# Kernel tuning notes

Hardware: AMD Instinct MI355X
Metric: run time of the kernel (lower is better)

Reference implementation:

```python
import jax, jax.numpy as jnp
import numpy as np
from jax import lax

B, S, F, D, H, L, A = 16, 512, 64, 512, 8, 4, 3
E = D // H  # head_dim = 64

def _gelu(t):
    return jax.nn.gelu(t, approximate=False)  # torch nn.GELU() is exact erf

def _make_masks():
    i = jnp.arange(S)[:, None]
    j = jnp.arange(S)[None, :]
    d = jnp.abs(i - j)
    ms = []
    for h in range(min(5, H)):
        dil = 2 ** h
        ms.append((d <= dil) | (d % (2 ** (h + 1)) == 0))
    m = jnp.stack(ms)  # [5,S,S] bool
    idx = jnp.minimum(jnp.arange(H), m.shape[0] - 1)
    return m[idx]  # [H,S,S]

MASKS = _make_masks()

def _ln(x, g, b, eps=1e-5):
    mu = jnp.mean(x, -1, keepdims=True)
    var = jnp.mean((x - mu) ** 2, -1, keepdims=True)
    return (x - mu) * lax.rsqrt(var + eps) * g + b

def _conv1d(x_ncw, w, b):
    y = lax.conv_general_dilated(x_ncw, w, (1,), [(1, 1)],
                                 dimension_numbers=("NCH", "OIH", "NCH"))
    return y + b[None, :, None]

def _attn(x, Wq, bq, Wk, bk, Wv, bv, Wo, bo):
    # x: [B,S,D]; Wq/Wk/Wv: [H,E,D] (stacked per-head Linear weights)
    q = jnp.einsum("bsd,hed->bhse", x, Wq) + bq[None, :, None, :]
    k = jnp.einsum("bsd,hed->bhse", x, Wk) + bk[None, :, None, :]
    v = jnp.einsum("bsd,hed->bhse", x, Wv) + bv[None, :, None, :]
    s = jnp.einsum("bhse,bhte->bhst", q, k) / (E ** 0.5)
    s = jnp.where(MASKS[None], s, -jnp.inf)  # log-sparse masked_fill
    p = jax.nn.softmax(s, axis=-1)
    o = jnp.einsum("bhst,bhte->bhse", p, v)
    o = o.transpose(0, 2, 1, 3).reshape(x.shape[0], x.shape[1], D)  # concat heads
    return o @ Wo.T + bo

def _forward(x, conv1_w, conv1_b, conv2_w, conv2_b, emb_w, emb_b, pos,
             Wq, bq, Wk, bk, Wv, bv, Wo, bo, ln1_g, ln1_b, ln2_g, ln2_b,
             W1, b1, W2, b2, lnf_g, lnf_b,
             a1_w, a1_b, a2_w, a2_b, a3_w, a3_b, a4_w, a4_b,
             c1_w, c1_b, c2_w, c2_b, c3_w, c3_b, c4_w, c4_b):
    # feature extractor: two conv1d+GELU over time axis
    h0 = _gelu(_conv1d(x.transpose(0, 2, 1), conv1_w, conv1_b))
    h0 = _gelu(_conv1d(h0, conv2_w, conv2_b)).transpose(0, 2, 1)  # [B,S,D]
    z = h0 @ emb_w.T + emb_b + pos[:, :S]  # input embedding + positional
    for l in range(L):  # PyraFormer blocks (pre-norm residual)
        z = z + _attn(_ln(z, ln1_g[l], ln1_b[l]),
                      Wq[l], bq[l], Wk[l], bk[l], Wv[l], bv[l], Wo[l], bo[l])
        h = _ln(z, ln2_g[l], ln2_b[l])
        z = z + (_gelu(h @ W1[l].T + b1[l]) @ W2[l].T + b2[l])
    z = _ln(z, lnf_g, lnf_b)
    feat = z[:, -1, :]  # last timestep features

    def head(f, layers):
        (w1, bb1), (w2, bb2), (w3, bb3), (w4, bb4) = layers
        f = _gelu(f @ w1.T + bb1)
        f = _gelu(f @ w2.T + bb2)
        f = _gelu(f @ w3.T + bb3)
        return f @ w4.T + bb4

    policy = head(feat, [(a1_w, a1_b), (a2_w, a2_b), (a3_w, a3_b), (a4_w, a4_b)])
    value = head(feat, [(c1_w, c1_b), (c2_w, c2_b), (c3_w, c3_b), (c4_w, c4_b)])
    return policy, value

def setup_inputs() -> dict:
    key = jax.random.key(0)
    ks = iter(jax.random.split(key, 64))
    r = lambda shape, s=0.05: jax.random.normal(next(ks), shape, jnp.float32) * s
    return {
        "x": jax.random.normal(next(ks), (B, S, F), jnp.float32),
        "conv1_w": r((D // 2, F, 3)), "conv1_b": jnp.zeros((D // 2,)),
        "conv2_w": r((D, D // 2, 3)), "conv2_b": jnp.zeros((D,)),
        "emb_w": r((D, D)), "emb_b": jnp.zeros((D,)),
        "pos": r((1, S, D), 0.02),
        "Wq": r((L, H, E, D)), "bq": jnp.zeros((L, H, E)),
        "Wk": r((L, H, E, D)), "bk": jnp.zeros((L, H, E)),
        "Wv": r((L, H, E, D)), "bv": jnp.zeros((L, H, E)),
        "Wo": r((L, D, D)), "bo": jnp.zeros((L, D)),
        "ln1_g": jnp.ones((L, D)), "ln1_b": jnp.zeros((L, D)),
        "ln2_g": jnp.ones((L, D)), "ln2_b": jnp.zeros((L, D)),
        "W1": r((L, 4 * D, D)), "b1": jnp.zeros((L, 4 * D)),
        "W2": r((L, D, 4 * D)), "b2": jnp.zeros((L, D)),
        "lnf_g": jnp.ones((D,)), "lnf_b": jnp.zeros((D,)),
        "a1_w": r((128, D)), "a1_b": jnp.zeros((128,)),
        "a2_w": r((256, 128)), "a2_b": jnp.zeros((256,)),
        "a3_w": r((57, 256)), "a3_b": jnp.zeros((57,)),
        "a4_w": r((A, 57)), "a4_b": jnp.zeros((A,)),
        "c1_w": r((128, D)), "c1_b": jnp.zeros((128,)),
        "c2_w": r((256, 128)), "c2_b": jnp.zeros((256,)),
        "c3_w": r((57, 256)), "c3_b": jnp.zeros((57,)),
        "c4_w": r((1, 57)), "c4_b": jnp.zeros((1,)),
    }

def reference(x, conv1_w, conv1_b, conv2_w, conv2_b, emb_w, emb_b, pos,
              Wq, bq, Wk, bk, Wv, bv, Wo, bo, ln1_g, ln1_b, ln2_g, ln2_b,
              W1, b1, W2, b2, lnf_g, lnf_b,
              a1_w, a1_b, a2_w, a2_b, a3_w, a3_b, a4_w, a4_b,
              c1_w, c1_b, c2_w, c2_b, c3_w, c3_b, c4_w, c4_b):
    return _forward(x, conv1_w, conv1_b, conv2_w, conv2_b, emb_w, emb_b, pos,
                    Wq, bq, Wk, bk, Wv, bv, Wo, bo, ln1_g, ln1_b, ln2_g, ln2_b,
                    W1, b1, W2, b2, lnf_g, lnf_b,
                    a1_w, a1_b, a2_w, a2_b, a3_w, a3_b, a4_w, a4_b,
                    c1_w, c1_b, c2_w, c2_b, c3_w, c3_b, c4_w, c4_b)
```

## Files before the change

### kernel.cpp

```cpp
#include <hip/hip_runtime.h>
#include <hip/hip_bf16.h>
#include <cstdint>

typedef __attribute__((ext_vector_type(8))) short bf16x8;
typedef __attribute__((ext_vector_type(4))) float f32x4;
typedef unsigned short u16;

#define DEV __device__ __forceinline__

DEV float b2f(u16 u) {
  union { unsigned int i; float f; } v; v.i = ((unsigned int)u) << 16; return v.f;
}
DEV u16 f2b(float f) {
  __hip_bfloat16 h = __float2bfloat16(f);
  return *reinterpret_cast<u16*>(&h);
}
DEV float erf_fast(float x) {
  float ax = fabsf(x);
  float t = __builtin_amdgcn_rcpf(fmaf(0.3275911f, ax, 1.0f));
  float p = t * fmaf(t, fmaf(t, fmaf(t, fmaf(t, 1.061405429f, -1.453152027f),
                                     1.421413741f), -0.284496736f), 0.254829592f);
  float r = fmaf(-p, __expf(-ax * ax), 1.0f);
  return copysignf(r, x);
}
DEV float gelu_f(float x) { return 0.5f * x * (1.0f + erf_fast(x * 0.70710678118654752f)); }

DEV void async_cp16(const u16* g, u16* l) {
  __builtin_amdgcn_global_load_lds(
      (const __attribute__((address_space(1))) void*)g,
      (__attribute__((address_space(3))) void*)l, 16, 0, 0);
}

__global__ void probe_kernel(const unsigned int* __restrict__ g, int* __restrict__ flag) {
  if (threadIdx.x == 0 && blockIdx.x == 0) *flag = (*g == 0x3F800000u) ? 1 : 0;
}

struct CvtArgs {
  const void* src[42];
  unsigned int off[43];
};

struct alignas(16) U8v { u16 u[8]; };
struct alignas(8)  U4v { u16 u[4]; };

__global__ __launch_bounds__(256) void cvt_kernel(CvtArgs a, int n_t, unsigned int total,
                                                  const int* __restrict__ flag,
                                                  u16* __restrict__ dst) {
  unsigned int i8 = (blockIdx.x * 256u + threadIdx.x) * 8u;
  if (i8 >= total) return;
  int t = 0;
  while (t + 1 < n_t && i8 >= a.off[t + 1]) t++;
  unsigned int j = i8 - a.off[t];
  bool in_seg = (i8 + 8 <= a.off[t + 1]) && (i8 + 8 <= total);
  int fp32 = *flag;
  if (fp32) {
    if (in_seg && ((j & 3) == 0)) {
      const float* s = (const float*)a.src[t] + j;
      float4 v0 = *(const float4*)s;
      float4 v1 = *(const float4*)(s + 4);
      U8v o;
      o.u[0] = f2b(v0.x); o.u[1] = f2b(v0.y); o.u[2] = f2b(v0.z); o.u[3] = f2b(v0.w);
      o.u[4] = f2b(v1.x); o.u[5] = f2b(v1.y); o.u[6] = f2b(v1.z); o.u[7] = f2b(v1.w);
      *(U8v*)(dst + i8) = o;
    } else {
      for (int k = 0; k < 8; k++) {
        unsigned int i = i8 + k;
        if (i >= total) break;
        int tt = t;
        while (tt + 1 < n_t && i >= a.off[tt + 1]) tt++;
        dst[i] = f2b(((const float*)a.src[tt])[i - a.off[tt]]);
      }
    }
  } else {
    if (in_seg && ((j & 7) == 0)) {
      *(U8v*)(dst + i8) = *(const U8v*)((const u16*)a.src[t] + j);
    } else {
      for (int k = 0; k < 8; k++) {
        unsigned int i = i8 + k;
        if (i >= total) break;
        int tt = t;
        while (tt + 1 < n_t && i >= a.off[tt + 1]) tt++;
        dst[i] = ((const u16*)a.src[tt])[i - a.off[tt]];
      }
    }
  }
}

__global__ __launch_bounds__(256) void gemm_bt44(
    const u16* __restrict__ A, const u16* __restrict__ W,
    const u16* __restrict__ bias,
    u16* __restrict__ outB, float* __restrict__ outF,
    const u16* __restrict__ pos,
    int N, int K, int mode)
{
  __shared__ __align__(16) u16 As[2][64 * 32];
  __shared__ __align__(16) u16 Bs[2][64 * 32];
  int t = threadIdx.x, l = t & 63, w = t >> 6;
  int wr = w >> 1, wc = w & 1;
  int col = l & 15, quad = l >> 4;
  int q8 = (quad ^ ((col >> 1) & 3)) * 8;
  int m0 = blockIdx.x * 64;
  int n0 = blockIdx.y * 64;

  f32x4 acc[2][2];
#pragma unroll
  for (int i = 0; i < 2; i++)
#pragma unroll
    for (int j = 0; j < 2; j++) acc[i][j] = (f32x4){0.f, 0.f, 0.f, 0.f};

  int ra = t >> 2;
  int ca = (t & 3) ^ ((ra >> 1) & 3);
  const u16* a1 = A + (size_t)(m0 + ra) * K + ca * 8;
  const u16* b1 = W + (size_t)(n0 + ra) * K + ca * 8;

  int nK = K >> 5;
  async_cp16(a1, &As[0][t * 8]);
  async_cp16(b1, &Bs[0][t * 8]);
  for (int ki = 0; ki < nK; ki++) {
    int cur = ki & 1;
    if (ki + 1 < nK) {
      int nxt = cur ^ 1, kt = (ki + 1) << 5;
      async_cp16(a1 + kt, &As[nxt][t * 8]);
      async_cp16(b1 + kt, &Bs[nxt][t * 8]);
      __builtin_amdgcn_s_waitcnt(0x0F72);
    } else {
      __builtin_amdgcn_s_waitcnt(0x0F70);
    }
    __builtin_amdgcn_s_barrier();
    __builtin_amdgcn_sched_barrier(0);
    bf16x8 af[2], bfv[2];
#pragma unroll
    for (int mi = 0; mi < 2; mi++)
      af[mi] = *(const bf16x8*)&As[cur][(wr * 32 + mi * 16 + col) * 32 + q8];
#pragma unroll
    for (int ni = 0; ni < 2; ni++)
      bfv[ni] = *(const bf16x8*)&Bs[cur][(wc * 32 + ni * 16 + col) * 32 + q8];
#pragma unroll
    for (int mi = 0; mi < 2; mi++)
#pragma unroll
      for (int ni = 0; ni < 2; ni++)
        acc[mi][ni] = __builtin_amdgcn_mfma_f32_16x16x32_bf16(bfv[ni], af[mi], acc[mi][ni], 0, 0, 0);
    __builtin_amdgcn_sched_barrier(0);
    __builtin_amdgcn_s_barrier();
  }

  int mBase = m0 + wr * 32, nBase = n0 + wc * 32;
  if (mode == 1) {
#pragma unroll
    for (int mi = 0; mi < 2; mi++) {
      int m = mBase + mi * 16 + col;
      size_t rowOff = (size_t)m * N;
#pragma unroll
      for (int ni = 0; ni < 2; ni++) {
        int n4 = nBase + ni * 16 + quad * 4;
        U4v bb = *(const U4v*)&bias[n4];
        f32x4 v = acc[mi][ni];
        U4v o;
#pragma unroll
        for (int r = 0; r < 4; r++) o.u[r] = f2b(gelu_f(v[r] + b2f(bb.u[r])));
        *(U4v*)&outB[rowOff + n4] = o;
      }
    }
  } else if (mode == 2) {
#pragma unroll
    for (int mi = 0; mi < 2; mi++) {
      int m = mBase + mi * 16 + col;
      size_t rowOff = (size_t)m * N;
#pragma unroll
      for (int ni = 0; ni < 2; ni++) {
        int n4 = nBase + ni * 16 + quad * 4;
        U4v bb = *(const U4v*)&bias[n4];
        f32x4 v = acc[mi][ni];
        float4* p = (float4*)&outF[rowOff + n4];
        float4 zv = *p;
        zv.x += v[0] + b2f(bb.u[0]);
        zv.y += v[1] + b2f(bb.u[1]);
        zv.z += v[2] + b2f(bb.u[2]);
        zv.w += v[3] + b2f(bb.u[3]);
        *p = zv;
      }
    }
  } else {
#pragma unroll
    for (int mi = 0; mi < 2; mi++) {
      int m = mBase + mi * 16 + col;
      int s = m & 511;
      size_t rowOff = (size_t)m * N;
#pragma unroll
      for (int ni = 0; ni < 2; ni++) {
        int n4 = nBase + ni * 16 + quad * 4;
        U4v bb = *(const U4v*)&bias[n4];
        U4v pp = *(const U4v*)&pos[s * 512 + n4];
        f32x4 v = acc[mi][ni];
        float4 zv;
        zv.x = v[0] + b2f(bb.u[0]) + b2f(pp.u[0]);
        zv.y = v[1] + b2f(bb.u[1]) + b2f(pp.u[1]);
        zv.z = v[2] + b2f(bb.u[2]) + b2f(pp.u[2]);
        zv.w = v[3] + b2f(bb.u[3]) + b2f(pp.u[3]);
        *(float4*)&outF[rowOff + n4] = zv;
      }
    }
  }
}

__global__ __launch_bounds__(256) void gemm_bt128x64(
    const u16* __restrict__ A, const u16* __restrict__ W,
    const u16* __restrict__ bias,
    u16* __restrict__ outB, int N, int K)
{
  __shared__ __align__(16) u16 As[2][128 * 32];
  __shared__ __align__(16) u16 Bs[2][64 * 32];
  int t = threadIdx.x, l = t & 63, w = t >> 6;
  int wr = w >> 1, wc = w & 1;
  int col = l & 15, quad = l >> 4;
  int q8 = (quad ^ ((col >> 1) & 3)) * 8;
  int m0 = blockIdx.x * 128;
  int n0 = blockIdx.y * 64;

  f32x4 acc[4][2];
#pragma unroll
  for (int i = 0; i < 4; i++)
#pragma unroll
    for (int j = 0; j < 2; j++) acc[i][j] = (f32x4){0.f, 0.f, 0.f, 0.f};

  int g1i = t, g2i = t + 256;
  int r1 = g1i >> 2, r2 = g2i >> 2;
  int cb1 = (g1i & 3) ^ ((r1 >> 1) & 3);
  int cb2 = (g2i & 3) ^ ((r2 >> 1) & 3);
  int rb = t >> 2;
  int cbb = (t & 3) ^ ((rb >> 1) & 3);
  const u16* a1 = A + (size_t)(m0 + r1) * K + cb1 * 8;
  const u16* a2 = A + (size_t)(m0 + r2) * K + cb2 * 8;
  const u16* b1 = W + (size_t)(n0 + rb) * K + cbb * 8;

  int nK = K >> 5;
  async_cp16(a1, &As[0][g1i * 8]);
  async_cp16(a2, &As[0][g2i * 8]);
  async_cp16(b1, &Bs[0][t * 8]);
  for (int ki = 0; ki < nK; ki++) {
    int cur = ki & 1;
    if (ki + 1 < nK) {
      int nxt = cur ^ 1, kt = (ki + 1) << 5;
      async_cp16(a1 + kt, &As[nxt][g1i * 8]);
      async_cp16(a2 + kt, &As[nxt][g2i * 8]);
      async_cp16(b1 + kt, &Bs[nxt][t * 8]);
      __builtin_amdgcn_s_waitcnt(0x0F73);
    } else {
      __builtin_amdgcn_s_waitcnt(0x0F70);
    }
    __builtin_amdgcn_s_barrier();
    __builtin_amdgcn_sched_barrier(0);
    bf16x8 af[4], bfv[2];
#pragma unroll
    for (int mi = 0; mi < 4; mi++)
      af[mi] = *(const bf16x8*)&As[cur][(wr * 64 + mi * 16 + col) * 32 + q8];
#pragma unroll
    for (int ni = 0; ni < 2; ni++)
      bfv[ni] = *(const bf16x8*)&Bs[cur][(wc * 32 + ni * 16 + col) * 32 + q8];
#pragma unroll
    for (int mi = 0; mi < 4; mi++)
#pragma unroll
      for (int ni = 0; ni < 2; ni++)
        acc[mi][ni] = __builtin_amdgcn_mfma_f32_16x16x32_bf16(bfv[ni], af[mi], acc[mi][ni], 0, 0, 0);
    __builtin_amdgcn_sched_barrier(0);
    __builtin_amdgcn_s_barrier();
  }

  int mBase = m0 + wr * 64, nBase = n0 + wc * 32;
#pragma unroll
  for (int mi = 0; mi < 4; mi++) {
    int m = mBase + mi * 16 + col;
    size_t rowOff = (size_t)m * N;
#pragma unroll
    for (int ni = 0; ni < 2; ni++) {
      int n4 = nBase + ni * 16 + quad * 4;
      U4v bb = *(const U4v*)&bias[n4];
      f32x4 v = acc[mi][ni];
      U4v o;
#pragma unroll
      for (int r = 0; r < 4; r++) o.u[r] = f2b(gelu_f(v[r] + b2f(bb.u[r])));
      *(U4v*)&outB[rowOff + n4] = o;
    }
  }
}

__global__ __launch_bounds__(256) void gemm_qkv256(
    const u16* __restrict__ A,
    const u16* __restrict__ Wq, const u16* __restrict__ Wk, const u16* __restrict__ Wv,
    const u16* __restrict__ bq, const u16* __restrict__ bk, const u16* __restrict__ bv,
    u16* __restrict__ outQ, u16* __restrict__ outK, u16* __restrict__ outVT, int K)
{
  __shared__ __align__(16) u16 As[2][64 * 32];
  __shared__ __align__(16) u16 Bs[2][256 * 32];
  int t = threadIdx.x, l = t & 63, w = t >> 6;
  int wr = w >> 1, wc = w & 1;
  int col = l & 15, quad = l >> 4;
  int q8 = (quad ^ ((col >> 1) & 3)) * 8;
  int m0 = blockIdx.x * 64;
  int sel = blockIdx.y >> 1;
  int n0 = (blockIdx.y & 1) * 256;
  const u16* W = sel == 0 ? Wq : (sel == 1 ? Wk : Wv);
  const u16* bias = sel == 0 ? bq : (sel == 1 ? bk : bv);
  const bool swp = (sel < 2);
  const float scl = sel == 0 ? 0.125f : 1.0f;

  f32x4 acc[2][8];
#pragma unroll
  for (int i = 0; i < 2; i++)
#pragma unroll
    for (int j = 0; j < 8; j++) acc[i][j] = (f32x4){0.f, 0.f, 0.f, 0.f};

  int ra = t >> 2;
  int ca = (t & 3) ^ ((ra >> 1) & 3);
  const u16* a1 = A + (size_t)(m0 + ra) * K + ca * 8;
  const u16* bptr[4];
  int bidx[4];
#pragma unroll
  for (int j = 0; j < 4; j++) {
    int gi = t + 256 * j;
    int rb = gi >> 2;
    int cb = (gi & 3) ^ ((rb >> 1) & 3);
    bptr[j] = W + (size_t)(n0 + rb) * K + cb * 8;
    bidx[j] = gi;
  }

  int nK = K >> 5;
  async_cp16(a1, &As[0][t * 8]);
#pragma unroll
  for (int j = 0; j < 4; j++) async_cp16(bptr[j], &Bs[0][bidx[j] * 8]);
  for (int ki = 0; ki < nK; ki++) {
    int cur = ki & 1;
    if (ki + 1 < nK) {
      int nxt = cur ^ 1, kt = (ki + 1) << 5;
      async_cp16(a1 + kt, &As[nxt][t * 8]);
#pragma unroll
      for (int j = 0; j < 4; j++) async_cp16(bptr[j] + kt, &Bs[nxt][bidx[j] * 8]);
      __builtin_amdgcn_s_waitcnt(0x0F75);
    } else {
      __builtin_amdgcn_s_waitcnt(0x0F70);
    }
    __builtin_amdgcn_s_barrier();
    __builtin_amdgcn_sched_barrier(0);
    bf16x8 af[2], bfv[8];
#pragma unroll
    for (int mi = 0; mi < 2; mi++)
      af[mi] = *(const bf16x8*)&As[cur][(wr * 32 + mi * 16 + col) * 32 + q8];
#pragma unroll
    for (int ni = 0; ni < 8; ni++)
      bfv[ni] = *(const bf16x8*)&Bs[cur][(wc * 128 + ni * 16 + col) * 32 + q8];
    if (swp) {
#pragma unroll
      for (int mi = 0; mi < 2; mi++)
#pragma unroll
        for (int ni = 0; ni < 8; ni++)
          acc[mi][ni] = __builtin_amdgcn_mfma_f32_16x16x32_bf16(bfv[ni], af[mi], acc[mi][ni], 0, 0, 0);
    } else {
#pragma unroll
      for (int mi = 0; mi < 2; mi++)
#pragma unroll
        for (int ni = 0; ni < 8; ni++)
          acc[mi][ni] = __builtin_amdgcn_mfma_f32_16x16x32_bf16(af[mi], bfv[ni], acc[mi][ni], 0, 0, 0);
    }
    __builtin_amdgcn_sched_barrier(0);
    __builtin_amdgcn_s_barrier();
  }

  int mBase = m0 + wr * 32, nBase = n0 + wc * 128;
  if (swp) {
    u16* outB = sel == 0 ? outQ : outK;
#pragma unroll
    for (int mi = 0; mi < 2; mi++) {
      int m = mBase + mi * 16 + col;
      size_t rowOff = (size_t)m * 512;
#pragma unroll
      for (int ni = 0; ni < 8; ni++) {
        int n4 = nBase + ni * 16 + quad * 4;
        U4v bb = *(const U4v*)&bias[n4];
        f32x4 v = acc[mi][ni];
        U4v o;
#pragma unroll
        for (int r = 0; r < 4; r++) o.u[r] = f2b((v[r] + b2f(bb.u[r])) * scl);
        *(U4v*)&outB[rowOff + n4] = o;
      }
    }
  } else {
    int b = m0 >> 9;
    int sB = m0 & 511;
#pragma unroll
    for (int mi = 0; mi < 2; mi++) {
      int s4 = sB + wr * 32 + mi * 16 + quad * 4;
#pragma unroll
      for (int ni = 0; ni < 8; ni++) {
        int n = nBase + ni * 16 + col;
        int h = n >> 6, e = n & 63;
        float bvv = b2f(bias[n]);
        f32x4 v = acc[mi][ni];
        U4v o;
#pragma unroll
        for (int r = 0; r < 4; r++) o.u[r] = f2b(v[r] + bvv);
        *(U4v*)&outVT[((size_t)((b * 8 + h) * 64 + e)) * 512 + s4] = o;
      }
    }
  }
}

__global__ void im2col3_kernel(const u16* __restrict__ src,
                               u16* __restrict__ dst, int C)
{
  int m = blockIdx.x;
  int k = blockIdx.y * blockDim.x + threadIdx.x;
  int ci = k / 3;
  int tap = k - ci * 3;
  int s = m & 511;
  int sp = s + tap - 1;
  u16 val = 0;
  if (sp >= 0 && sp < 512) val = src[(size_t)(m + tap - 1) * C + ci];
  dst[(size_t)m * (3 * C) + k] = val;
}

__global__ __launch_bounds__(256) void ln_kernel(
    const float* __restrict__ z, const u16* __restrict__ gam,
    const u16* __restrict__ bet, u16* __restrict__ out)
{
  int w = threadIdx.x >> 6, l = threadIdx.x & 63;
  int row = blockIdx.x * 4 + w;
  const float* zr = z + (size_t)row * 512;
  float4 v0 = *(const float4*)(zr + l * 8);
  float4 v1 = *(const float4*)(zr + l * 8 + 4);
  float x[8] = {v0.x, v0.y, v0.z, v0.w, v1.x, v1.y, v1.z, v1.w};
  float s = 0.f;
#pragma unroll
  for (int i = 0; i < 8; i++) s += x[i];
#pragma unroll
  for (int mm = 1; mm < 64; mm <<= 1) s += __shfl_xor(s, mm, 64);
  float mu = s * (1.0f / 512.0f);
  float vs = 0.f;
#pragma unroll
  for (int i = 0; i < 8; i++) { float d = x[i] - mu; vs += d * d; }
#pragma unroll
  for (int mm = 1; mm < 64; mm <<= 1) vs += __shfl_xor(vs, mm, 64);
  float rs = rsqrtf(vs * (1.0f / 512.0f) + 1e-5f);
  U8v gg = *(const U8v*)(gam + l * 8);
  U8v bb = *(const U8v*)(bet + l * 8);
  U8v o;
#pragma unroll
  for (int i = 0; i < 8; i++) o.u[i] = f2b((x[i] - mu) * rs * b2f(gg.u[i]) + b2f(bb.u[i]));
  *(U8v*)(out + (size_t)row * 512 + l * 8) = o;
}

__global__ __launch_bounds__(256) void lnf_kernel(
    const float* __restrict__ z, const u16* __restrict__ gam,
    const u16* __restrict__ bet, u16* __restrict__ feat)
{
  int w = threadIdx.x >> 6, l = threadIdx.x & 63;
  int b = blockIdx.x * 4 + w;
  const float* zr = z + ((size_t)b * 512 + 511) * 512;
  float4 v0 = *(const float4*)(zr + l * 8);
  float4 v1 = *(const float4*)(zr + l * 8 + 4);
  float x[8] = {v0.x, v0.y, v0.z, v0.w, v1.x, v1.y, v1.z, v1.w};
  float s = 0.f;
#pragma unroll
  for (int i = 0; i < 8; i++) s += x[i];
#pragma unroll
  for (int mm = 1; mm < 64; mm <<= 1) s += __shfl_xor(s, mm, 64);
  float mu = s * (1.0f / 512.0f);
  float vs = 0.f;
#pragma unroll
  for (int i = 0; i < 8; i++) { float d = x[i] - mu; vs += d * d; }
#pragma unroll
  for (int mm = 1; mm < 64; mm <<= 1) vs += __shfl_xor(vs, mm, 64);
  float rs = rsqrtf(vs * (1.0f / 512.0f) + 1e-5f);
  U8v gg = *(const U8v*)(gam + l * 8);
  U8v bb = *(const U8v*)(bet + l * 8);
  U8v o;
#pragma unroll
  for (int i = 0; i < 8; i++) o.u[i] = f2b((x[i] - mu) * rs * b2f(gg.u[i]) + b2f(bb.u[i]));
  *(U8v*)(feat + (size_t)b * 512 + l * 8) = o;
}

#define AST 72
__global__ __launch_bounds__(256) void attn_kernel(
    const u16* __restrict__ Q, const u16* __restrict__ Kg,
    const u16* __restrict__ VT, u16* __restrict__ O)
{
  __shared__ __align__(16) u16 Ks[64 * AST];
  __shared__ __align__(16) u16 Vts[64 * AST];
  __shared__ __align__(16) u16 Ps[64 * AST];
  const float NEG = -1e30f;
  int blk = blockIdx.x;
  int bh = blk & 127;
  int i0 = (blk >> 7) * 64;
  int b = bh >> 3, h = bh & 7;
  int t = threadIdx.x, w = t >> 6, l = t & 63;
  int col = l & 15, quad = l >> 4;
  int dil = 1 << (h < 4 ? h : 4);
  int per_m1 = 2 * dil - 1;

  {
    int row = t >> 2, c = (t & 3) * 16;
    const u16* src = Q + ((size_t)(b * 512 + i0 + row) * 512 + h * 64 + c);
    *(float4*)&Ps[row * AST + c] = *(const float4*)src;
    *(float4*)&Ps[row * AST + c + 8] = *(const float4*)(src + 8);
  }
  __builtin_amdgcn_s_waitcnt(0xC07F);
  __builtin_amdgcn_sched_barrier(0);
  bf16x8 qa[2];
#pragma unroll
  for (int kk = 0; kk < 2; kk++)
    qa[kk] = *(const bf16x8*)&Ps[(w * 16 + col) * AST + kk * 32 + quad * 8];

  f32x4 acc_o[4];
#pragma unroll
  for (int i = 0; i < 4; i++) acc_o[i] = (f32x4){0.f, 0.f, 0.f, 0.f};
  float m_run = NEG, l_run = 0.f;
  int ig = i0 + w * 16 + col;

  for (int jt = 0; jt < 8; jt++) {
    int j0 = jt * 64;
    {
      int row = t >> 2, c = (t & 3) * 16;
      const u16* ks = Kg + ((size_t)(b * 512 + j0 + row) * 512 + h * 64 + c);
      *(float4*)&Ks[row * AST + c] = *(const float4*)ks;
      *(float4*)&Ks[row * AST + c + 8] = *(const float4*)(ks + 8);
      const u16* vs = VT + ((size_t)(bh * 64 + row) * 512 + j0 + c);
      *(float4*)&Vts[row * AST + c] = *(const float4*)vs;
      *(float4*)&Vts[row * AST + c + 8] = *(const float4*)(vs + 8);
    }
    __syncthreads();

    f32x4 sa[4];
    __builtin_amdgcn_s_setprio(1);
#pragma unroll
    for (int ni = 0; ni < 4; ni++) {
      f32x4 s = (f32x4){0.f, 0.f, 0.f, 0.f};
#pragma unroll
      for (int kk = 0; kk < 2; kk++) {
        bf16x8 kb = *(const bf16x8*)&Ks[(ni * 16 + col) * AST + kk * 32 + quad * 8];
        s = __builtin_amdgcn_mfma_f32_16x16x32_bf16(kb, qa[kk], s, 0, 0, 0);
      }
      sa[ni] = s;
    }
    __builtin_amdgcn_s_setprio(0);

    float mx = NEG;
#pragma unroll
    for (int ni = 0; ni < 4; ni++)
#pragma unroll
      for (int r = 0; r < 4; r++) {
        int jg = j0 + ni * 16 + quad * 4 + r;
        int d = ig - jg; d = d < 0 ? -d : d;
        bool keep = (d <= dil) || ((d & per_m1) == 0);
        float s = keep ? sa[ni][r] : NEG;
        sa[ni][r] = s;
        mx = fmaxf(mx, s);
      }
    mx = fmaxf(mx, __shfl_xor(mx, 16, 64));
    mx = fmaxf(mx, __shfl_xor(mx, 32, 64));
    float mN = fmaxf(m_run, mx);
    float alpha = __expf(m_run - mN);
    m_run = mN;
    float rsum = 0.f;
#pragma unroll
    for (int ni = 0; ni < 4; ni++)
#pragma unroll
      for (int r = 0; r < 4; r++) {
        float p = __expf(sa[ni][r] - mN);
        sa[ni][r] = p;
        rsum += p;
      }
    rsum += __shfl_xor(rsum, 16, 64);
    rsum += __shfl_xor(rsum, 32, 64);
    l_run = l_run * alpha + rsum;

#pragma unroll
    for (int ni = 0; ni < 4; ni++) {
      unsigned int lo = (unsigned int)f2b(sa[ni][0]) | ((unsigned int)f2b(sa[ni][1]) << 16);
      unsigned int hi = (unsigned int)f2b(sa[ni][2]) | ((unsigned int)f2b(sa[ni][3]) << 16);
      uint2 pk; pk.x = lo; pk.y = hi;
      *(uint2*)&Ps[(w * 16 + col) * AST + ni * 16 + quad * 4] = pk;
    }
    __builtin_amdgcn_s_waitcnt(0xC07F);
    __builtin_amdgcn_sched_barrier(0);

    float a_sh[4];
#pragma unroll
    for (int r = 0; r < 4; r++) a_sh[r] = __shfl(alpha, quad * 4 + r, 64);
#pragma unroll
    for (int ne = 0; ne < 4; ne++)
#pragma unroll
      for (int r = 0; r < 4; r++) acc_o[ne][r] *= a_sh[r];

    bf16x8 pa[2];
#pragma unroll
    for (int kk = 0; kk < 2; kk++)
      pa[kk] = *(const bf16x8*)&Ps[(w * 16 + col) * AST + kk * 32 + quad * 8];
    __builtin_amdgcn_s_setprio(1);
#pragma unroll
    for (int ne = 0; ne < 4; ne++) {
#pragma unroll
      for (int kk = 0; kk < 2; kk++) {
        bf16x8 vb = *(const bf16x8*)&Vts[(ne * 16 + col) * AST + kk * 32 + quad * 8];
        acc_o[ne] = __builtin_amdgcn_mfma_f32_16x16x32_bf16(pa[kk], vb, acc_o[ne], 0, 0, 0);
      }
    }
    __builtin_amdgcn_s_setprio(0);
    __syncthreads();
  }

  float inv[4];
#pragma unroll
  for (int r = 0; r < 4; r++) {
    float lr = __shfl(l_run, quad * 4 + r, 64);
    inv[r] = 1.0f / fmaxf(lr, 1e-20f);
  }
#pragma unroll
  for (int ne = 0; ne < 4; ne++)
#pragma unroll
    for (int r = 0; r < 4; r++) {
      float o = acc_o[ne][r] * inv[r];
      O[((size_t)(b * 512 + i0 + w * 16 + quad * 4 + r)) * 512 + h * 64 + ne * 16 + col] = f2b(o);
    }
}

__global__ __launch_bounds__(256) void heads_kernel(
    const u16* __restrict__ feat,
    const u16* __restrict__ a1w, const u16* __restrict__ a1b,
    const u16* __restrict__ a2w, const u16* __restrict__ a2b,
    const u16* __restrict__ a3w, const u16* __restrict__ a3b,
    const u16* __restrict__ a4w, const u16* __restrict__ a4b,
    const u16* __restrict__ c1w, const u16* __restrict__ c1b,
    const u16* __restrict__ c2w, const u16* __restrict__ c2b,
    const u16* __restrict__ c3w, const u16* __restrict__ c3b,
    const u16* __restrict__ c4w, const u16* __restrict__ c4b,
    const int* __restrict__ flag, void* __restrict__ outv)
{
  __shared__ float f[512];
  __shared__ float g1[256];
  __shared__ float g2[512];
  __shared__ float g3[128];
  int b = blockIdx.x, t = threadIdx.x;
  f[t] = b2f(feat[b * 512 + t]);
  f[t + 256] = b2f(feat[b * 512 + 256 + t]);
  __syncthreads();
  {
    const u16* wrow; float bias;
    if (t < 128) { wrow = a1w + (size_t)t * 512; bias = b2f(a1b[t]); }
    else { wrow = c1w + (size_t)(t - 128) * 512; bias = b2f(c1b[t - 128]); }
    float s = bias;
    for (int k = 0; k < 512; k += 8) {
      U8v wv = *(const U8v*)(wrow + k);
#pragma unroll
      for (int j = 0; j < 8; j++) s += b2f(wv.u[j]) * f[k + j];
    }
    g1[t] = gelu_f(s);
  }
  __syncthreads();
  {
    float s1 = b2f(a2b[t]);
    for (int k = 0; k < 128; k += 8) {
      U8v wv = *(const U8v*)(a2w + (size_t)t * 128 + k);
#pragma unroll
      for (int j = 0; j < 8; j++) s1 += b2f(wv.u[j]) * g1[k + j];
    }
    float s2 = b2f(c2b[t]);
    for (int k = 0; k < 128; k += 8) {
      U8v wv = *(const U8v*)(c2w + (size_t)t * 128 + k);
#pragma unroll
      for (int j = 0; j < 8; j++) s2 += b2f(wv.u[j]) * g1[128 + k + j];
    }
    g2[t] = gelu_f(s1);
    g2[256 + t] = gelu_f(s2);
  }
  __syncthreads();
  if (t < 57) {
    float s = b2f(a3b[t]);
    for (int k = 0; k < 256; k += 8) {
      U8v wv = *(const U8v*)(a3w + (size_t)t * 256 + k);
#pragma unroll
      for (int j = 0; j < 8; j++) s += b2f(wv.u[j]) * g2[k + j];
    }
    g3[t] = gelu_f(s);
  } else if (t >= 64 && t < 121) {
    int u = t - 64;
    float s = b2f(c3b[u]);
    for (int k = 0; k < 256; k += 8) {
      U8v wv = *(const U8v*)(c3w + (size_t)u * 256 + k);
#pragma unroll
      for (int j = 0; j < 8; j++) s += b2f(wv.u[j]) * g2[256 + k + j];
    }
    g3[64 + u] = gelu_f(s);
  }
  __syncthreads();
  int fp32out = *flag;
  if (t < 3) {
    float s = b2f(a4b[t]);
    for (int k = 0; k < 57; k++) s += b2f(a4w[t * 57 + k]) * g3[k];
    if (fp32out) ((float*)outv)[b * 3 + t] = s;
    else ((u16*)outv)[b * 3 + t] = f2b(s);
  } else if (t == 4) {
    float s = b2f(c4b[0]);
    for (int k = 0; k < 57; k++) s += b2f(c4w[k]) * g3[64 + k];
    if (fp32out) ((float*)outv)[48 + b] = s;
    else ((u16*)outv)[48 + b] = f2b(s);
  }
}

extern "C" void kernel_launch(void* const* d_in, const int* in_sizes, int n_in,
                              void* d_out, int out_size, void* d_ws, size_t ws_size,
                              hipStream_t stream)
{
  char* ws = (char*)d_ws;
  float* z    = (float*)ws;
  u16* R      = (u16*)(ws + (16u << 20));
  u16* bufQ   = R;
  u16* bufK   = (u16*)(ws + (24u << 20));
  u16* bufO   = (u16*)(ws + (32u << 20));
  u16* bufVT  = (u16*)(ws + (40u << 20));
  u16* bufH   = (u16*)(ws + (48u << 20));
  u16* feat   = R;
  u16* pool   = (u16*)(ws + (56u << 20));
  int* flag   = (int*)(ws + (88u << 20));

  CvtArgs args;
  unsigned int off = 0;
  int nt = n_in < 42 ? n_in : 42;
  for (int i = 0; i < nt; i++) { args.src[i] = d_in[i]; args.off[i] = off; off += (unsigned int)in_sizes[i]; }
  args.off[nt] = off;
  unsigned int total = off;

  probe_kernel<<<1, 64, 0, stream>>>((const unsigned int*)d_in[24], flag);
  cvt_kernel<<<(total + 2047) / 2048, 256, 0, stream>>>(args, nt, total, flag, pool);

  const u16* P[42];
  for (int i = 0; i < nt; i++) P[i] = pool + args.off[i];
  const u16* x       = P[0];
  const u16* conv1_w = P[1];  const u16* conv1_b = P[2];
  const u16* conv2_w = P[3];  const u16* conv2_b = P[4];
  const u16* emb_w   = P[5];  const u16* emb_b   = P[6];
  const u16* pos     = P[7];
  const u16* Wq      = P[8];  const u16* bq      = P[9];
  const u16* Wk      = P[10]; const u16* bk      = P[11];
  const u16* Wv      = P[12]; const u16* bv      = P[13];
  const u16* Wo      = P[14]; const u16* bo      = P[15];
  const u16* ln1_g   = P[16]; const u16* ln1_b   = P[17];
  const u16* ln2_g   = P[18]; const u16* ln2_b   = P[19];
  const u16* W1      = P[20]; const u16* b1      = P[21];
  const u16* W2      = P[22]; const u16* b2      = P[23];
  const u16* lnf_g   = P[24]; const u16* lnf_b   = P[25];

  im2col3_kernel<<<dim3(8192, 1), 192, 0, stream>>>(x, R, 64);
  gemm_bt44<<<dim3(128, 4), 256, 0, stream>>>(R, conv1_w, conv1_b, bufH, nullptr, nullptr, 256, 192, 1);
  im2col3_kernel<<<dim3(8192, 3), 256, 0, stream>>>(bufH, R, 256);
  gemm_bt44<<<dim3(128, 8), 256, 0, stream>>>(R, conv2_w, conv2_b, bufH, nullptr, nullptr, 512, 768, 1);
  gemm_bt44<<<dim3(128, 8), 256, 0, stream>>>(bufH, emb_w, emb_b, nullptr, z, pos, 512, 512, 4);

  for (int l = 0; l < 4; l++) {
    ln_kernel<<<2048, 256, 0, stream>>>(z, ln1_g + l * 512, ln1_b + l * 512, bufH);
    gemm_qkv256<<<dim3(128, 6), 256, 0, stream>>>(bufH,
        Wq + (size_t)l * 262144, Wk + (size_t)l * 262144, Wv + (size_t)l * 262144,
        bq + l * 512, bk + l * 512, bv + l * 512, bufQ, bufK, bufVT, 512);
    attn_kernel<<<dim3(1024), 256, 0, stream>>>(bufQ, bufK, bufVT, bufO);
    gemm_bt44<<<dim3(128, 8), 256, 0, stream>>>(bufO, Wo + (size_t)l * 262144, bo + l * 512, nullptr, z, nullptr, 512, 512, 2);
    ln_kernel<<<2048, 256, 0, stream>>>(z, ln2_g + l * 512, ln2_b + l * 512, bufH);
    gemm_bt128x64<<<dim3(64, 32), 256, 0, stream>>>(bufH, W1 + (size_t)l * 1048576, b1 + l * 2048, R, 2048, 512);
    gemm_bt44<<<dim3(128, 8), 256, 0, stream>>>(R, W2 + (size_t)l * 1048576, b2 + l * 512, nullptr, z, nullptr, 512, 2048, 2);
  }

  lnf_kernel<<<4, 256, 0, stream>>>(z, lnf_g, lnf_b, feat);
  heads_kernel<<<16, 256, 0, stream>>>(feat,
      P[26], P[27], P[28], P[29], P[30], P[31], P[32], P[33],
      P[34], P[35], P[36], P[37], P[38], P[39], P[40], P[41],
      flag, d_out);
}
```

Baseline: 913.6 us.

## Fold LayerNorm into GEMM epilogues via row stats and precomputed weight sums

Removes the standalone LayerNorm kernels. Each residual-producing GEMM epilogue now writes z scaled by gamma in bf16 and atomically accumulates per-row sum and sum-of-squares. The consuming QKV and FFN1 GEMMs then apply mean/rstd correction using vectors W·gamma and W·beta+bias, which a new kernel precomputes at the start of every call. This saves a full read/write pass over activations per LN, but adds atomics and a one-pass variance formula that can lose precision. It also adds a weight-preprocessing kernel to each call.

```diff
diff --git a/kernel.cpp b/kernel.cpp
--- a/kernel.cpp
+++ b/kernel.cpp
@@ -86,11 +86,70 @@
   }
 }
 
+__global__ __launch_bounds__(256) void xform_kernel(
+    const u16* __restrict__ Wq, const u16* __restrict__ Wk, const u16* __restrict__ Wv,
+    const u16* __restrict__ W1,
+    const u16* __restrict__ bq, const u16* __restrict__ bk, const u16* __restrict__ bv,
+    const u16* __restrict__ b1,
+    const u16* __restrict__ ln1_g, const u16* __restrict__ ln1_b,
+    const u16* __restrict__ ln2_g, const u16* __restrict__ ln2_b,
+    float* __restrict__ stats, float* __restrict__ cvec)
+{
+  int bid = blockIdx.x;
+  if (bid < 144) {
+    int i = (bid * 256 + threadIdx.x) * 4;
+    *(float4*)&stats[i] = (float4){0.f, 0.f, 0.f, 0.f};
+    return;
+  }
+  int rid = (bid - 144) * 4 + (threadIdx.x >> 6);
+  int l = rid / 3584;
+  int rr = rid - l * 3584;
+  const u16 *Wrow, *g, *b;
+  float bias;
+  float *c1p, *c2p;
+  float* cl = cvec + l * 7168;
+  if (rr < 1536) {
+    int sel = rr >> 9, row = rr & 511;
+    const u16* Wm = sel == 0 ? Wq : (sel == 1 ? Wk : Wv);
+    const u16* bm = sel == 0 ? bq : (sel == 1 ? bk : bv);
+    Wrow = Wm + (size_t)l * 262144 + (size_t)row * 512;
+    g = ln1_g + l * 512; b = ln1_b + l * 512;
+    bias = b2f(bm[l * 512 + row]);
+    c1p = cl + sel * 1024 + row;
+    c2p = cl + sel * 1024 + 512 + row;
+  } else {
+    int row = rr - 1536;
+    Wrow = W1 + (size_t)l * 1048576 + (size_t)row * 512;
+    g = ln2_g + l * 512; b = ln2_b + l * 512;
+    bias = b2f(b1[l * 2048 + row]);
+    c1p = cl + 3072 + row;
+    c2p = cl + 3072 + 2048 + row;
+  }
+  int lane = threadIdx.x & 63;
+  U8v wv = *(const U8v*)(Wrow + lane * 8);
+  U8v gv = *(const U8v*)(g + lane * 8);
+  U8v bv2 = *(const U8v*)(b + lane * 8);
+  float s1 = 0.f, s2 = 0.f;
+#pragma unroll
+  for (int j = 0; j < 8; j++) {
+    float w = b2f(wv.u[j]);
+    s1 += w * b2f(gv.u[j]);
+    s2 += w * b2f(bv2.u[j]);
+  }
+#pragma unroll
+  for (int mm = 1; mm < 64; mm <<= 1) {
+    s1 += __shfl_xor(s1, mm, 64);
+    s2 += __shfl_xor(s2, mm, 64);
+  }
+  if (lane == 0) { *c1p = s1; *c2p = s2 + bias; }
+}
+
 __global__ __launch_bounds__(256) void gemm_bt44(
     const u16* __restrict__ A, const u16* __restrict__ W,
     const u16* __restrict__ bias,
     u16* __restrict__ outB, float* __restrict__ outF,
     const u16* __restrict__ pos,
+    const u16* __restrict__ g_vec, float* __restrict__ stats, u16* __restrict__ zb,
     int N, int K, int mode)
 {
   __shared__ __align__(16) u16 As[2][64 * 32];
@@ -161,43 +220,47 @@
         *(U4v*)&outB[rowOff + n4] = o;
       }
     }
-  } else if (mode == 2) {
+  } else {
 #pragma unroll
     for (int mi = 0; mi < 2; mi++) {
       int m = mBase + mi * 16 + col;
       size_t rowOff = (size_t)m * N;
+      float s = 0.f, s2 = 0.f;
 #pragma unroll
       for (int ni = 0; ni < 2; ni++) {
         int n4 = nBase + ni * 16 + quad * 4;
         U4v bb = *(const U4v*)&bias[n4];
         f32x4 v = acc[mi][ni];
-        float4* p = (float4*)&outF[rowOff + n4];
-        float4 zv = *p;
-        zv.x += v[0] + b2f(bb.u[0]);
-        zv.y += v[1] + b2f(bb.u[1]);
-        zv.z += v[2] + b2f(bb.u[2]);
-        zv.w += v[3] + b2f(bb.u[3]);
-        *p = zv;
-      }
-    }
-  } else {
-#pragma unroll
-    for (int mi = 0; mi < 2; mi++) {
-      int m = mBase + mi * 16 + col;
-      int s = m & 511;
-      size_t rowOff = (size_t)m * N;
-#pragma unroll
-      for (int ni = 0; ni < 2; ni++) {
-        int n4 = nBase + ni * 16 + quad * 4;
-        U4v bb = *(const U4v*)&bias[n4];
-        U4v pp = *(const U4v*)&pos[s * 512 + n4];
-        f32x4 v = acc[mi][ni];
         float4 zv;
-        zv.x = v[0] + b2f(bb.u[0]) + b2f(pp.u[0]);
-        zv.y = v[1] + b2f(bb.u[1]) + b2f(pp.u[1]);
-        zv.z = v[2] + b2f(bb.u[2]) + b2f(pp.u[2]);
-        zv.w = v[3] + b2f(bb.u[3]) + b2f(pp.u[3]);
+        if (mode == 2) {
+          float4 old = *(float4*)&outF[rowOff + n4];
+          zv.x = old.x + v[0] + b2f(bb.u[0]);
+          zv.y = old.y + v[1] + b2f(bb.u[1]);
+          zv.z = old.z + v[2] + b2f(bb.u[2]);
+          zv.w = old.w + v[3] + b2f(bb.u[3]);
+        } else {
+          U4v pp = *(const U4v*)&pos[(m & 511) * 512 + n4];
+          zv.x = v[0] + b2f(bb.u[0]) + b2f(pp.u[0]);
+          zv.y = v[1] + b2f(bb.u[1]) + b2f(pp.u[1]);
+          zv.z = v[2] + b2f(bb.u[2]) + b2f(pp.u[2]);
+          zv.w = v[3] + b2f(bb.u[3]) + b2f(pp.u[3]);
+        }
         *(float4*)&outF[rowOff + n4] = zv;
+        U4v gg = *(const U4v*)&g_vec[n4];
+        U4v ob;
+        ob.u[0] = f2b(zv.x * b2f(gg.u[0]));
+        ob.u[1] = f2b(zv.y * b2f(gg.u[1]));
+        ob.u[2] = f2b(zv.z * b2f(gg.u[2]));
+        ob.u[3] = f2b(zv.w * b2f(gg.u[3]));
+        *(U4v*)&zb[rowOff + n4] = ob;
+        s  += zv.x + zv.y + zv.z + zv.w;
+        s2 += zv.x * zv.x + zv.y * zv.y + zv.z * zv.z + zv.w * zv.w;
+      }
+      s  += __shfl_xor(s, 16, 64);  s  += __shfl_xor(s, 32, 64);
+      s2 += __shfl_xor(s2, 16, 64); s2 += __shfl_xor(s2, 32, 64);
+      if (quad == 0) {
+        atomicAdd(&stats[2 * m], s);
+        atomicAdd(&stats[2 * m + 1], s2);
       }
     }
   }
@@ -205,7 +268,8 @@
 
 __global__ __launch_bounds__(256) void gemm_bt128x64(
     const u16* __restrict__ A, const u16* __restrict__ W,
-    const u16* __restrict__ bias,
+    const float* __restrict__ stats,
+    const float* __restrict__ c1, const float* __restrict__ c2,
     u16* __restrict__ outB, int N, int K)
 {
   __shared__ __align__(16) u16 As[2][128 * 32];
@@ -271,14 +335,22 @@
   for (int mi = 0; mi < 4; mi++) {
     int m = mBase + mi * 16 + col;
     size_t rowOff = (size_t)m * N;
+    float st0 = stats[2 * m], st1 = stats[2 * m + 1];
+    float mu = st0 * (1.0f / 512.0f);
+    float var = st1 * (1.0f / 512.0f) - mu * mu;
+    float rs = rsqrtf(var + 1e-5f);
+    float nmu = rs * mu;
 #pragma unroll
     for (int ni = 0; ni < 2; ni++) {
       int n4 = nBase + ni * 16 + quad * 4;
-      U4v bb = *(const U4v*)&bias[n4];
+      float4 c1v = *(const float4*)&c1[n4];
+      float4 c2v = *(const float4*)&c2[n4];
       f32x4 v = acc[mi][ni];
       U4v o;
-#pragma unroll
-      for (int r = 0; r < 4; r++) o.u[r] = f2b(gelu_f(v[r] + b2f(bb.u[r])));
+      o.u[0] = f2b(gelu_f(rs * v[0] - nmu * c1v.x + c2v.x));
+      o.u[1] = f2b(gelu_f(rs * v[1] - nmu * c1v.y + c2v.y));
+      o.u[2] = f2b(gelu_f(rs * v[2] - nmu * c1v.z + c2v.z));
+      o.u[3] = f2b(gelu_f(rs * v[3] - nmu * c1v.w + c2v.w));
       *(U4v*)&outB[rowOff + n4] = o;
     }
   }
@@ -287,7 +359,7 @@
 __global__ __launch_bounds__(256) void gemm_qkv256(
     const u16* __restrict__ A,
     const u16* __restrict__ Wq, const u16* __restrict__ Wk, const u16* __restrict__ Wv,
-    const u16* __restrict__ bq, const u16* __restrict__ bk, const u16* __restrict__ bv,
+    const float* __restrict__ stats, const float* __restrict__ cv,
     u16* __restrict__ outQ, u16* __restrict__ outK, u16* __restrict__ outVT, int K)
 {
   __shared__ __align__(16) u16 As[2][64 * 32];
@@ -300,7 +372,8 @@
   int sel = blockIdx.y >> 1;
   int n0 = (blockIdx.y & 1) * 256;
   const u16* W = sel == 0 ? Wq : (sel == 1 ? Wk : Wv);
-  const u16* bias = sel == 0 ? bq : (sel == 1 ? bk : bv);
+  const float* c1 = cv + sel * 1024;
+  const float* c2 = c1 + 512;
   const bool swp = (sel < 2);
   const float scl = sel == 0 ? 0.125f : 1.0f;
 
@@ -372,14 +445,22 @@
     for (int mi = 0; mi < 2; mi++) {
       int m = mBase + mi * 16 + col;
       size_t rowOff = (size_t)m * 512;
+      float st0 = stats[2 * m], st1 = stats[2 * m + 1];
+      float mu = st0 * (1.0f / 512.0f);
+      float var = st1 * (1.0f / 512.0f) - mu * mu;
+      float rs = rsqrtf(var + 1e-5f);
+      float nmu = rs * mu;
 #pragma unroll
       for (int ni = 0; ni < 8; ni++) {
         int n4 = nBase + ni * 16 + quad * 4;
-        U4v bb = *(const U4v*)&bias[n4];
+        float4 c1v = *(const float4*)&c1[n4];
+        float4 c2v = *(const float4*)&c2[n4];
         f32x4 v = acc[mi][ni];
         U4v o;
-#pragma unroll
-        for (int r = 0; r < 4; r++) o.u[r] = f2b((v[r] + b2f(bb.u[r])) * scl);
+        o.u[0] = f2b((rs * v[0] - nmu * c1v.x + c2v.x) * scl);
+        o.u[1] = f2b((rs * v[1] - nmu * c1v.y + c2v.y) * scl);
+        o.u[2] = f2b((rs * v[2] - nmu * c1v.z + c2v.z) * scl);
+        o.u[3] = f2b((rs * v[3] - nmu * c1v.w + c2v.w) * scl);
         *(U4v*)&outB[rowOff + n4] = o;
       }
     }
@@ -388,16 +469,27 @@
     int sB = m0 & 511;
 #pragma unroll
     for (int mi = 0; mi < 2; mi++) {
+      int mb4 = m0 + wr * 32 + mi * 16 + quad * 4;
       int s4 = sB + wr * 32 + mi * 16 + quad * 4;
+      float rs_r[4], nmu_r[4];
+#pragma unroll
+      for (int r = 0; r < 4; r++) {
+        float st0 = stats[2 * (mb4 + r)], st1 = stats[2 * (mb4 + r) + 1];
+        float mu = st0 * (1.0f / 512.0f);
+        float var = st1 * (1.0f / 512.0f) - mu * mu;
+        float rs = rsqrtf(var + 1e-5f);
+        rs_r[r] = rs; nmu_r[r] = rs * mu;
+      }
 #pragma unroll
       for (int ni = 0; ni < 8; ni++) {
         int n = nBase + ni * 16 + col;
         int h = n >> 6, e = n & 63;
-        float bvv = b2f(bias[n]);
+        float c1s = c1[n], c2s = c2[n];
         f32x4 v = acc[mi][ni];
         U4v o;
 #pragma unroll
-        for (int r = 0; r < 4; r++) o.u[r] = f2b(v[r] + bvv);
+        for (int r = 0; r < 4; r++)
+          o.u[r] = f2b(rs_r[r] * v[r] - nmu_r[r] * c1s + c2s);
         *(U4v*)&outVT[((size_t)((b * 8 + h) * 64 + e)) * 512 + s4] = o;
       }
     }
@@ -416,36 +508,6 @@
   u16 val = 0;
   if (sp >= 0 && sp < 512) val = src[(size_t)(m + tap - 1) * C + ci];
   dst[(size_t)m * (3 * C) + k] = val;
-}
-
-__global__ __launch_bounds__(256) void ln_kernel(
-    const float* __restrict__ z, const u16* __restrict__ gam,
-    const u16* __restrict__ bet, u16* __restrict__ out)
-{
-  int w = threadIdx.x >> 6, l = threadIdx.x & 63;
-  int row = blockIdx.x * 4 + w;
-  const float* zr = z + (size_t)row * 512;
-  float4 v0 = *(const float4*)(zr + l * 8);
-  float4 v1 = *(const float4*)(zr + l * 8 + 4);
-  float x[8] = {v0.x, v0.y, v0.z, v0.w, v1.x, v1.y, v1.z, v1.w};
-  float s = 0.f;
-#pragma unroll
-  for (int i = 0; i < 8; i++) s += x[i];
-#pragma unroll
-  for (int mm = 1; mm < 64; mm <<= 1) s += __shfl_xor(s, mm, 64);
-  float mu = s * (1.0f / 512.0f);
-  float vs = 0.f;
-#pragma unroll
-  for (int i = 0; i < 8; i++) { float d = x[i] - mu; vs += d * d; }
-#pragma unroll
-  for (int mm = 1; mm < 64; mm <<= 1) vs += __shfl_xor(vs, mm, 64);
-  float rs = rsqrtf(vs * (1.0f / 512.0f) + 1e-5f);
-  U8v gg = *(const U8v*)(gam + l * 8);
-  U8v bb = *(const U8v*)(bet + l * 8);
-  U8v o;
-#pragma unroll
-  for (int i = 0; i < 8; i++) o.u[i] = f2b((x[i] - mu) * rs * b2f(gg.u[i]) + b2f(bb.u[i]));
-  *(U8v*)(out + (size_t)row * 512 + l * 8) = o;
 }
 
 __global__ __launch_bounds__(256) void lnf_kernel(
@@ -715,10 +777,14 @@
   u16* bufQ   = R;
   u16* bufK   = (u16*)(ws + (24u << 20));
   u16* bufO   = (u16*)(ws + (32u << 20));
+  u16* bufC   = (u16*)(ws + (32u << 20));
   u16* bufVT  = (u16*)(ws + (40u << 20));
+  u16* zb     = (u16*)(ws + (48u << 20));
   u16* bufH   = (u16*)(ws + (48u << 20));
   u16* feat   = R;
   u16* pool   = (u16*)(ws + (56u << 20));
+  float* stats = (float*)(ws + (84u << 20));
+  float* cvec  = (float*)(ws + (85u << 20));
   int* flag   = (int*)(ws + (88u << 20));
 
   CvtArgs args;
@@ -748,22 +814,32 @@
   const u16* W2      = P[22]; const u16* b2      = P[23];
   const u16* lnf_g   = P[24]; const u16* lnf_b   = P[25];
 
+  xform_kernel<<<3728, 256, 0, stream>>>(Wq, Wk, Wv, W1, bq, bk, bv, b1,
+      ln1_g, ln1_b, ln2_g, ln2_b, stats, cvec);
+
   im2col3_kernel<<<dim3(8192, 1), 192, 0, stream>>>(x, R, 64);
-  gemm_bt44<<<dim3(128, 4), 256, 0, stream>>>(R, conv1_w, conv1_b, bufH, nullptr, nullptr, 256, 192, 1);
+  gemm_bt44<<<dim3(128, 4), 256, 0, stream>>>(R, conv1_w, conv1_b, bufH, nullptr,
+      nullptr, nullptr, nullptr, nullptr, 256, 192, 1);
   im2col3_kernel<<<dim3(8192, 3), 256, 0, stream>>>(bufH, R, 256);
-  gemm_bt44<<<dim3(128, 8), 256, 0, stream>>>(R, conv2_w, conv2_b, bufH, nullptr, nullptr, 512, 768, 1);
-  gemm_bt44<<<dim3(128, 8), 256, 0, stream>>>(bufH, emb_w, emb_b, nullptr, z, pos, 512, 512, 4);
+  gemm_bt44<<<dim3(128, 8), 256, 0, stream>>>(R, conv2_w, conv2_b, bufC, nullptr,
+      nullptr, nullptr, nullptr, nullptr, 512, 768, 1);
+  gemm_bt44<<<dim3(128, 8), 256, 0, stream>>>(bufC, emb_w, emb_b, nullptr, z,
+      pos, ln1_g, stats, zb, 512, 512, 4);
 
   for (int l = 0; l < 4; l++) {
-    ln_kernel<<<2048, 256, 0, stream>>>(z, ln1_g + l * 512, ln1_b + l * 512, bufH);
-    gemm_qkv256<<<dim3(128, 6), 256, 0, stream>>>(bufH,
+    float* cl = cvec + l * 7168;
+    gemm_qkv256<<<dim3(128, 6), 256, 0, stream>>>(zb,
         Wq + (size_t)l * 262144, Wk + (size_t)l * 262144, Wv + (size_t)l * 262144,
-        bq + l * 512, bk + l * 512, bv + l * 512, bufQ, bufK, bufVT, 512);
+        stats + (size_t)(2 * l) * 16384, cl, bufQ, bufK, bufVT, 512);
     attn_kernel<<<dim3(1024), 256, 0, stream>>>(bufQ, bufK, bufVT, bufO);
-    gemm_bt44<<<dim3(128, 8), 256, 0, stream>>>(bufO, Wo + (size_t)l * 262144, bo + l * 512, nullptr, z, nullptr, 512, 512, 2);
-    ln_kernel<<<2048, 256, 0, stream>>>(z, ln2_g + l * 512, ln2_b + l * 512, bufH);
-    gemm_bt128x64<<<dim3(64, 32), 256, 0, stream>>>(bufH, W1 + (size_t)l * 1048576, b1 + l * 2048, R, 2048, 512);
-    gemm_bt44<<<dim3(128, 8), 256, 0, stream>>>(R, W2 + (size_t)l * 1048576, b2 + l * 512, nullptr, z, nullptr, 512, 2048, 2);
+    gemm_bt44<<<dim3(128, 8), 256, 0, stream>>>(bufO, Wo + (size_t)l * 262144,
+        bo + l * 512, nullptr, z, nullptr, ln2_g + l * 512,
+        stats + (size_t)(2 * l + 1) * 16384, zb, 512, 512, 2);
+    gemm_bt128x64<<<dim3(64, 32), 256, 0, stream>>>(zb, W1 + (size_t)l * 1048576,
+        stats + (size_t)(2 * l + 1) * 16384, cl + 3072, cl + 3072 + 2048, R, 2048, 512);
+    gemm_bt44<<<dim3(128, 8), 256, 0, stream>>>(R, W2 + (size_t)l * 1048576,
+        b2 + l * 512, nullptr, z, nullptr, ln1_g + (l < 3 ? (l + 1) : 3) * 512,
+        stats + (size_t)(2 * l + 2) * 16384, zb, 512, 2048, 2);
   }
 
   lnf_kernel<<<4, 256, 0, stream>>>(z, lnf_g, lnf_b, feat);
```

Result: no change. 924.8 us (+1.2%).
